# Kernel optimization log

Hardware: AMD Instinct MI355X
Metric: run time of the kernel (lower is better)

The kernel has to match this reference:

```python
import jax, jax.numpy as jnp
import numpy as np

N = 100_000      # nodes
E = 3_200_000    # directed edges (avg degree 32)
F_IN = 503
C = 32           # GATConv out_channels, heads=1
NEG_SLOPE = 0.2  # PyG GATConv default


def setup_inputs() -> dict:
    key = jax.random.key(0)
    ks = jax.random.split(key, 14)
    x = jax.random.normal(ks[0], (N, F_IN), jnp.float32)
    edge_index = jax.random.randint(ks[1], (2, E), 0, N)
    edge_weight = jax.random.uniform(ks[2], (E, 1), jnp.float32)
    input_mask = jnp.ones((N, 1), jnp.float32)
    # GATConv params (heads=1)
    W_src = jax.random.normal(ks[3], (C, F_IN), jnp.float32) * 0.02
    att_src = jax.random.normal(ks[4], (C,), jnp.float32) * 0.1
    att_dst = jax.random.normal(ks[5], (C,), jnp.float32) * 0.1
    att_edge = jax.random.normal(ks[6], (C,), jnp.float32) * 0.1
    W_edge = jax.random.normal(ks[7], (C, 1), jnp.float32) * 0.1
    bias_conv = jnp.zeros((C,), jnp.float32)
    # dense heads
    Wb = jax.random.normal(ks[8], (1, C), jnp.float32) * 0.1
    bb = jnp.zeros((1,), jnp.float32)
    Ww = jax.random.normal(ks[9], (1, C), jnp.float32) * 0.1
    bw = jnp.zeros((1,), jnp.float32)
    return {"x": x, "edge_index": edge_index, "edge_weight": edge_weight,
            "input_mask": input_mask, "W_src": W_src, "att_src": att_src,
            "att_dst": att_dst, "att_edge": att_edge, "W_edge": W_edge,
            "bias_conv": bias_conv, "Wb": Wb, "bb": bb, "Ww": Ww, "bw": bw}


def reference(x, edge_index, edge_weight, input_mask, W_src, att_src, att_dst,
              att_edge, W_edge, bias_conv, Wb, bb, Ww, bw):
    n = x.shape[0]
    xl = x @ W_src.T                       # [N, C] transformed node features
    a_src = xl @ att_src                   # [N] per-node source attention logit
    a_dst = xl @ att_dst                   # [N]
    src, dst = edge_index[0], edge_index[1]
    # add_self_loops=True with fill_value='mean' for edge_attr (PyG default)
    loop = jnp.arange(n)
    mean_attr = jnp.mean(edge_weight, axis=0, keepdims=True)      # [1,1]
    ea = jnp.concatenate([edge_weight, jnp.broadcast_to(mean_attr, (n, 1))], 0)
    s = jnp.concatenate([src, loop])       # [E+N]
    d = jnp.concatenate([dst, loop])
    a_edge = (ea @ W_edge.T) @ att_edge    # [E+N]
    alpha = jax.nn.leaky_relu(a_src[s] + a_dst[d] + a_edge, NEG_SLOPE)
    # softmax over incoming edges of each destination node
    amax = jax.ops.segment_max(alpha, d, num_segments=n)
    ex = jnp.exp(alpha - amax[d])
    denom = jax.ops.segment_sum(ex, d, num_segments=n)
    w = ex / denom[d]                      # [E+N] attention coeffs
    msg = xl[s] * w[:, None]               # [E+N, C]
    out = jax.ops.segment_sum(msg, d, num_segments=n) + bias_conv  # [N, C]
    h = jax.nn.relu(out)
    biases = (h @ Wb.T + bb) * input_mask  # [N, 1]
    weights = ((h[src] + h[dst]) * 0.5) @ Ww.T + bw  # [E, 1]
    return weights, biases
```

## Files before the change

### kernel.cpp

```cpp
#include <hip/hip_runtime.h>
#include <stdint.h>

#define NN 100000
#define NE 3200000
#define FIN 503
#define COUT 32
#define NSLOPE 0.2f

#define BSH 6
#define NB 1563
#define HB 256
#define EPB (NE / HB)
#define MAXBE 2560

typedef __bf16 bf16x8 __attribute__((ext_vector_type(8)));
typedef float  f32x4  __attribute__((ext_vector_type(4)));

__device__ __forceinline__ unsigned short bf1(float f) {
    unsigned u = __float_as_uint(f);
    u = (u + 0x7FFFu + ((u >> 16) & 1u)) >> 16;
    return (unsigned short)u;
}
__device__ __forceinline__ unsigned bf2(float a, float b) {
    return (unsigned)bf1(a) | ((unsigned)bf1(b) << 16);
}
__device__ __forceinline__ float unbf(unsigned short h) {
    return __uint_as_float(((unsigned)h) << 16);
}

__global__ void k_wprep(const float* __restrict__ W, uint4* __restrict__ wfrag)
{
    int entry = blockIdx.x * 256 + threadIdx.x;
    if (entry >= 2048) return;
    int c = entry & 31;
    int quad = (entry >> 5) & 3;
    int chunk = entry >> 7;
    int kb = chunk * 32 + quad * 8;
    float v[8];
    #pragma unroll
    for (int j = 0; j < 8; ++j) {
        int k = kb + j;
        v[j] = (k < FIN) ? W[c * FIN + k] : 0.f;
    }
    uint4 o;
    o.x = bf2(v[0], v[1]); o.y = bf2(v[2], v[3]);
    o.z = bf2(v[4], v[5]); o.w = bf2(v[6], v[7]);
    wfrag[entry] = o;
}

#define GR 64

__global__ __launch_bounds__(256)
void k_gemm(const float* __restrict__ x, const uint4* __restrict__ wfrag,
            unsigned short* __restrict__ xlb)
{
    __shared__ __align__(16) unsigned short os[GR * 40];
    const int t = threadIdx.x;
    const int wv = t >> 6, lane = t & 63;
    const int m16 = lane & 15, quad = lane >> 4;
    const int row0 = blockIdx.x * GR;
    const int row = row0 + wv * 16 + m16;
    const int rowc = (row < NN) ? row : (NN - 1);
    const float* xr = x + (size_t)rowc * FIN;

    f32x4 acc0 = {0.f, 0.f, 0.f, 0.f};
    f32x4 acc1 = {0.f, 0.f, 0.f, 0.f};

    #pragma unroll 5
    for (int ch = 0; ch < 15; ++ch) {
        const int kb = ch * 32 + quad * 8;
        float av[8];
        #pragma unroll
        for (int j = 0; j < 8; ++j) av[j] = xr[kb + j];
        bf16x8 af;
        #pragma unroll
        for (int j = 0; j < 8; ++j) af[j] = (__bf16)av[j];
        uint4 b0 = wfrag[ch * 128 + quad * 32 + m16];
        uint4 b1 = wfrag[ch * 128 + quad * 32 + 16 + m16];
        acc0 = __builtin_amdgcn_mfma_f32_16x16x32_bf16(af, *(bf16x8*)&b0, acc0, 0, 0, 0);
        acc1 = __builtin_amdgcn_mfma_f32_16x16x32_bf16(af, *(bf16x8*)&b1, acc1, 0, 0, 0);
    }
    {
        const int kb = 480 + quad * 8;
        float av[8];
        #pragma unroll
        for (int j = 0; j < 8; ++j) av[j] = (kb + j < FIN) ? xr[kb + j] : 0.f;
        bf16x8 af;
        #pragma unroll
        for (int j = 0; j < 8; ++j) af[j] = (__bf16)av[j];
        uint4 b0 = wfrag[15 * 128 + quad * 32 + m16];
        uint4 b1 = wfrag[15 * 128 + quad * 32 + 16 + m16];
        acc0 = __builtin_amdgcn_mfma_f32_16x16x32_bf16(af, *(bf16x8*)&b0, acc0, 0, 0, 0);
        acc1 = __builtin_amdgcn_mfma_f32_16x16x32_bf16(af, *(bf16x8*)&b1, acc1, 0, 0, 0);
    }

    #pragma unroll
    for (int r = 0; r < 4; ++r) {
        int rr = wv * 16 + quad * 4 + r;
        os[rr * 40 + m16]      = bf1(acc0[r]);
        os[rr * 40 + 16 + m16] = bf1(acc1[r]);
    }
    __syncthreads();
    {
        int r = t >> 2, c0 = (t & 3) * 8;
        int grow = row0 + r;
        if (grow < NN) {
            uint4 o = *(const uint4*)&os[r * 40 + c0];
            *(uint4*)&xlb[(size_t)grow * COUT + c0] = o;
        }
    }
}

__global__ void k_attn(const unsigned short* __restrict__ xlb,
                       const float* __restrict__ att_s, const float* __restrict__ att_d,
                       float* __restrict__ a_src, float* __restrict__ a_dst)
{
    int n = blockIdx.x * 256 + threadIdx.x;
    if (n >= NN) return;
    const unsigned short* r = xlb + (size_t)n * COUT;
    float s = 0.f, d = 0.f;
    #pragma unroll
    for (int c = 0; c < COUT; c += 2) {
        unsigned u = *(const unsigned*)&r[c];
        float v0 = __uint_as_float(u << 16);
        float v1 = __uint_as_float(u & 0xFFFF0000u);
        s += v0 * att_s[c] + v1 * att_s[c + 1];
        d += v0 * att_d[c] + v1 * att_d[c + 1];
    }
    a_src[n] = s; a_dst[n] = d;
}

__global__ void k_stats(const float* __restrict__ ew, const float* __restrict__ W_edge,
                        const float* __restrict__ att_e, float* __restrict__ stats)
{
    float s = 0.f;
    for (int i = blockIdx.x * blockDim.x + threadIdx.x; i < NE; i += gridDim.x * blockDim.x)
        s += ew[i];
    #pragma unroll
    for (int off = 32; off > 0; off >>= 1) s += __shfl_xor(s, off);
    if ((threadIdx.x & 63) == 0) atomicAdd(&stats[0], s);
    if (blockIdx.x == 0 && threadIdx.x == 0) {
        float k = 0.f;
        for (int c = 0; c < COUT; ++c) k += W_edge[c] * att_e[c];
        stats[1] = k;
    }
}

__global__ __launch_bounds__(512)
void k_hist(const int* __restrict__ ei_dst, unsigned* __restrict__ part)
{
    __shared__ unsigned h[NB];
    for (int i = threadIdx.x; i < NB; i += 512) h[i] = 0u;
    __syncthreads();
    const int base = blockIdx.x * EPB;
    for (int i = threadIdx.x; i < EPB; i += 512)
        atomicAdd(&h[ei_dst[base + i] >> BSH], 1u);
    __syncthreads();
    for (int i = threadIdx.x; i < NB; i += 512)
        part[(size_t)blockIdx.x * NB + i] = h[i];
}

__global__ void k_colscan(unsigned* __restrict__ part, unsigned* __restrict__ colsum)
{
    __shared__ unsigned sm[HB];
    const int t = threadIdx.x;
    const int bkt = blockIdx.x;
    unsigned v = part[(size_t)t * NB + bkt];
    sm[t] = v;
    for (int off = 1; off < HB; off <<= 1) {
        __syncthreads();
        unsigned tv = (t >= off) ? sm[t - off] : 0u;
        __syncthreads();
        sm[t] += tv;
    }
    __syncthreads();
    part[(size_t)t * NB + bkt] = sm[t] - v;
    if (t == HB - 1) colsum[bkt] = sm[t];
}

__global__ void k_bscan(const unsigned* __restrict__ colsum, unsigned* __restrict__ bbase)
{
    __shared__ unsigned sm[256];
    __shared__ unsigned carry;
    const int t = threadIdx.x;
    if (t == 0) carry = 0u;
    __syncthreads();
    for (int c0 = 0; c0 < NB; c0 += 256) {
        int i = c0 + t;
        unsigned v = (i < NB) ? colsum[i] : 0u;
        sm[t] = v;
        for (int off = 1; off < 256; off <<= 1) {
            __syncthreads();
            unsigned tv = (t >= off) ? sm[t - off] : 0u;
            __syncthreads();
            sm[t] += tv;
        }
        __syncthreads();
        if (i < NB) bbase[i] = carry + sm[t] - v;
        __syncthreads();
        if (t == 0) carry += sm[255];
        __syncthreads();
    }
    if (t == 0) bbase[NB] = carry;
}

__global__ __launch_bounds__(512)
void k_scatter(const int* __restrict__ ei, const float* __restrict__ ew,
               const float* __restrict__ a_src, const float* __restrict__ stats,
               const unsigned* __restrict__ part, const unsigned* __restrict__ bbase,
               uint2* __restrict__ csr)
{
    __shared__ unsigned cur[NB];
    const int b = blockIdx.x;
    for (int i = threadIdx.x; i < NB; i += 512)
        cur[i] = bbase[i] + part[(size_t)b * NB + i];
    __syncthreads();
    const float kc = stats[1];
    const int base = b * EPB;
    for (int i = threadIdx.x; i < EPB; i += 512) {
        int e = base + i;
        int s = ei[e];
        int d = ei[NE + e];
        float pre = a_src[s] + kc * ew[e];
        unsigned pos = atomicAdd(&cur[d >> BSH], 1u);
        csr[pos] = make_uint2((unsigned)s | ((unsigned)(d & 63) << 20),
                              __float_as_uint(pre));
    }
}

__global__ __launch_bounds__(256)
void k_aggr(const uint2* __restrict__ csr, const unsigned* __restrict__ bbase,
            const float* __restrict__ a_src, const float* __restrict__ a_dst,
            const unsigned short* __restrict__ xlb, const float* __restrict__ stats,
            const float* __restrict__ bias_conv, const float* __restrict__ Wb,
            const float* __restrict__ bb, const float* __restrict__ Ww,
            const float* __restrict__ mask, float* __restrict__ out_b,
            float* __restrict__ hw)
{
    __shared__ uint2 rec[MAXBE];
    __shared__ unsigned seg[65], cur[64];
    const int t = threadIdx.x;
    const int b = blockIdx.x;
    const int jb = (int)bbase[b];
    int ne = (int)bbase[b + 1] - jb;
    if (ne > MAXBE) ne = MAXBE;

    if (t < 64) cur[t] = 0u;
    __syncthreads();
    for (int i = t; i < ne; i += 256)
        atomicAdd(&cur[csr[jb + i].x >> 20], 1u);
    __syncthreads();
    if (t < 64) {
        unsigned v = cur[t];
        unsigned s = v;
        #pragma unroll
        for (int off = 1; off < 64; off <<= 1) {
            unsigned u = __shfl_up(s, off, 64);
            if (t >= off) s += u;
        }
        seg[t + 1] = s;
        cur[t] = s - v;
        if (t == 0) seg[0] = 0u;
    }
    __syncthreads();
    for (int i = t; i < ne; i += 256) {
        uint2 r = csr[jb + i];
        unsigned pos = atomicAdd(&cur[r.x >> 20], 1u);
        rec[pos] = r;
    }
    __syncthreads();

    const float kmean = stats[1] * (stats[0] * (1.f / NE));
    const int lane = t & 31;
    for (int dl = t >> 5; dl < 64; dl += 8) {
        int d = (b << BSH) + dl;
        if (d >= NN) continue;
        const float adv = a_dst[d];
        float a0 = a_src[d] + adv + kmean;
        a0 = (a0 > 0.f) ? a0 : NSLOPE * a0;
        const float ps = __expf(a0);
        float l = 0.f;
        float acc = ps * unbf(xlb[(size_t)d * COUT + lane]);
        const int j0 = (int)seg[dl], j1 = (int)seg[dl + 1];
        for (int tb = j0; tb < j1; tb += 32) {
            int j = tb + lane;
            float p = 0.f;
            if (j < j1) {
                uint2 en = rec[j];
                float a = __uint_as_float(en.y) + adv;
                a = (a > 0.f) ? a : NSLOPE * a;
                p = __expf(a);
                rec[j].y = __float_as_uint(p);
            }
            l += p;
            int cnte = min(32, j1 - tb);
            #pragma unroll 4
            for (int k = 0; k < cnte; ++k) {
                uint2 en = rec[tb + k];
                acc += __uint_as_float(en.y) *
                       unbf(xlb[(size_t)(en.x & 0xFFFFFu) * COUT + lane]);
            }
        }
        #pragma unroll
        for (int off = 16; off > 0; off >>= 1) l += __shfl_xor(l, off, 32);
        l += ps;
        float h = fmaxf(acc / l + bias_conv[lane], 0.f);
        float pb = h * Wb[lane];
        float pw = h * Ww[lane];
        #pragma unroll
        for (int off = 16; off > 0; off >>= 1) {
            pb += __shfl_xor(pb, off, 32);
            pw += __shfl_xor(pw, off, 32);
        }
        if (lane == 0) {
            out_b[d] = (pb + bb[0]) * mask[d];
            hw[d] = pw;
        }
    }
}

__global__ void k_weights(const int* __restrict__ ei, const float* __restrict__ hw,
                          const float* __restrict__ bw, float* __restrict__ out_w)
{
    int e = blockIdx.x * 256 + threadIdx.x;
    if (e < NE) {
        int s = ei[e], d = ei[NE + e];
        out_w[e] = 0.5f * (hw[s] + hw[d]) + bw[0];
    }
}

extern "C" void kernel_launch(void* const* d_in, const int* in_sizes, int n_in,
                              void* d_out, int out_size, void* d_ws, size_t ws_size,
                              hipStream_t stream)
{
    const float* x        = (const float*)d_in[0];
    const int*   ei       = (const int*)d_in[1];
    const float* ew       = (const float*)d_in[2];
    const float* mask     = (const float*)d_in[3];
    const float* W_src    = (const float*)d_in[4];
    const float* att_src  = (const float*)d_in[5];
    const float* att_dst  = (const float*)d_in[6];
    const float* att_edge = (const float*)d_in[7];
    const float* W_edge   = (const float*)d_in[8];
    const float* bias_c   = (const float*)d_in[9];
    const float* Wb       = (const float*)d_in[10];
    const float* bb       = (const float*)d_in[11];
    const float* Ww       = (const float*)d_in[12];
    const float* bw       = (const float*)d_in[13];
    (void)in_sizes; (void)n_in; (void)out_size; (void)ws_size;

    char* wsp = (char*)d_ws;
    size_t off = 0;
    auto alloc = [&](size_t bytes) -> void* {
        void* p = wsp + off;
        off = (off + bytes + 255) & ~(size_t)255;
        return p;
    };
    unsigned short* xlb    = (unsigned short*)alloc((size_t)NN * COUT * 2);
    uint4*    wfrag  = (uint4*)alloc(2048 * 16);
    float*    a_src  = (float*)alloc((size_t)NN * 4);
    float*    a_dst  = (float*)alloc((size_t)NN * 4);
    float*    stats  = (float*)alloc(256);
    unsigned* part   = (unsigned*)alloc((size_t)HB * NB * 4);
    unsigned* colsum = (unsigned*)alloc((size_t)NB * 4);
    unsigned* bbase  = (unsigned*)alloc((size_t)(NB + 1) * 4);
    uint2*    csr    = (uint2*)alloc((size_t)NE * 8);
    float*    hw     = (float*)alloc((size_t)NN * 4);

    float* out_w = (float*)d_out;
    float* out_b = out_w + NE;

    hipMemsetAsync(stats, 0, 8, stream);

    k_wprep   <<<8, 256, 0, stream>>>(W_src, wfrag);
    k_gemm    <<<(NN + GR - 1) / GR, 256, 0, stream>>>(x, wfrag, xlb);
    k_attn    <<<(NN + 255) / 256, 256, 0, stream>>>(xlb, att_src, att_dst, a_src, a_dst);
    k_stats   <<<1024, 256, 0, stream>>>(ew, W_edge, att_edge, stats);
    k_hist    <<<HB, 512, 0, stream>>>(ei + NE, part);
    k_colscan <<<NB, HB, 0, stream>>>(part, colsum);
    k_bscan   <<<1, 256, 0, stream>>>(colsum, bbase);
    k_scatter <<<HB, 512, 0, stream>>>(ei, ew, a_src, stats, part, bbase, csr);
    k_aggr    <<<NB, 256, 0, stream>>>(csr, bbase, a_src, a_dst, xlb, stats,
                                       bias_c, Wb, bb, Ww, mask, out_b, hw);
    k_weights <<<NE / 256, 256, 0, stream>>>(ei, hw, bw, out_w);
}
```

Before: 583.8 us.

## Fuse prep kernels, stage GEMM input through LDS, register-cache CSR records

Merges weight-fragment prep into the edge-weight reduction kernel, which now writes per-block partial sums instead of using atomics and a memset. The final reduction and the attention constant move into the single-block bucket scan. The node-attention dot products are folded into the GEMM epilogue, and GEMM input rows are staged through shared memory with coalesced loads. The aggregation kernel keeps its CSR records in registers instead of reading them twice. The goal is fewer launches and less redundant global traffic, at the cost of extra barriers in the GEMM loop and more register pressure in the aggregation kernel.

Measured after the change: 530.9 us. 1.1x faster.

```diff
diff --git a/kernel.cpp b/kernel.cpp
--- a/kernel.cpp
+++ b/kernel.cpp
@@ -12,6 +12,7 @@
 #define HB 256
 #define EPB (NE / HB)
 #define MAXBE 2560
+#define NREG (MAXBE / 256)
 
 typedef __bf16 bf16x8 __attribute__((ext_vector_type(8)));
 typedef float  f32x4  __attribute__((ext_vector_type(4)));
@@ -28,50 +29,78 @@
     return __uint_as_float(((unsigned)h) << 16);
 }
 
-__global__ void k_wprep(const float* __restrict__ W, uint4* __restrict__ wfrag)
-{
-    int entry = blockIdx.x * 256 + threadIdx.x;
-    if (entry >= 2048) return;
-    int c = entry & 31;
-    int quad = (entry >> 5) & 3;
-    int chunk = entry >> 7;
-    int kb = chunk * 32 + quad * 8;
-    float v[8];
+__global__ __launch_bounds__(256)
+void k_stats(const float* __restrict__ ew, float* __restrict__ partial,
+             const float* __restrict__ W, uint4* __restrict__ wfrag)
+{
+    const int t = threadIdx.x;
+    const int gid = blockIdx.x * 256 + t;
+
+    if (gid < 2048) {
+        int c = gid & 31;
+        int quad = (gid >> 5) & 3;
+        int chunk = gid >> 7;
+        int kb = chunk * 32 + quad * 8;
+        float v[8];
+        #pragma unroll
+        for (int j = 0; j < 8; ++j) {
+            int k = kb + j;
+            v[j] = (k < FIN) ? W[c * FIN + k] : 0.f;
+        }
+        uint4 o;
+        o.x = bf2(v[0], v[1]); o.y = bf2(v[2], v[3]);
+        o.z = bf2(v[4], v[5]); o.w = bf2(v[6], v[7]);
+        wfrag[gid] = o;
+    }
+
+    const float4* ew4 = (const float4*)ew;
+    float s = 0.f;
+    for (int i = gid; i < NE / 4; i += gridDim.x * 256) {
+        float4 v = ew4[i];
+        s += v.x + v.y + v.z + v.w;
+    }
     #pragma unroll
-    for (int j = 0; j < 8; ++j) {
-        int k = kb + j;
-        v[j] = (k < FIN) ? W[c * FIN + k] : 0.f;
-    }
-    uint4 o;
-    o.x = bf2(v[0], v[1]); o.y = bf2(v[2], v[3]);
-    o.z = bf2(v[4], v[5]); o.w = bf2(v[6], v[7]);
-    wfrag[entry] = o;
+    for (int off = 32; off > 0; off >>= 1) s += __shfl_xor(s, off);
+    __shared__ float wsum[4];
+    if ((t & 63) == 0) wsum[t >> 6] = s;
+    __syncthreads();
+    if (t == 0) partial[blockIdx.x] = wsum[0] + wsum[1] + wsum[2] + wsum[3];
 }
 
 #define GR 64
 
 __global__ __launch_bounds__(256)
 void k_gemm(const float* __restrict__ x, const uint4* __restrict__ wfrag,
-            unsigned short* __restrict__ xlb)
-{
+            const float* __restrict__ att_s, const float* __restrict__ att_d,
+            unsigned short* __restrict__ xlb,
+            float* __restrict__ a_src, float* __restrict__ a_dst)
+{
+    __shared__ __align__(16) float xs[GR][36];
     __shared__ __align__(16) unsigned short os[GR * 40];
     const int t = threadIdx.x;
     const int wv = t >> 6, lane = t & 63;
     const int m16 = lane & 15, quad = lane >> 4;
     const int row0 = blockIdx.x * GR;
-    const int row = row0 + wv * 16 + m16;
-    const int rowc = (row < NN) ? row : (NN - 1);
-    const float* xr = x + (size_t)rowc * FIN;
+    const int srow = t >> 5;
+    const int scol = t & 31;
 
     f32x4 acc0 = {0.f, 0.f, 0.f, 0.f};
     f32x4 acc1 = {0.f, 0.f, 0.f, 0.f};
-
-    #pragma unroll 5
-    for (int ch = 0; ch < 15; ++ch) {
-        const int kb = ch * 32 + quad * 8;
+    const int rowf = wv * 16 + m16;
+
+    for (int ch = 0; ch < 16; ++ch) {
+        const int k = ch * 32 + scol;
+        #pragma unroll
+        for (int p = 0; p < 8; ++p) {
+            int r = p * 8 + srow;
+            int rg = row0 + r;
+            rg = (rg < NN) ? rg : (NN - 1);
+            xs[r][scol] = (k < FIN) ? x[(size_t)rg * FIN + k] : 0.f;
+        }
+        __syncthreads();
         float av[8];
-        #pragma unroll
-        for (int j = 0; j < 8; ++j) av[j] = xr[kb + j];
+        *(f32x4*)&av[0] = *(const f32x4*)&xs[rowf][quad * 8];
+        *(f32x4*)&av[4] = *(const f32x4*)&xs[rowf][quad * 8 + 4];
         bf16x8 af;
         #pragma unroll
         for (int j = 0; j < 8; ++j) af[j] = (__bf16)av[j];
@@ -79,19 +108,7 @@
         uint4 b1 = wfrag[ch * 128 + quad * 32 + 16 + m16];
         acc0 = __builtin_amdgcn_mfma_f32_16x16x32_bf16(af, *(bf16x8*)&b0, acc0, 0, 0, 0);
         acc1 = __builtin_amdgcn_mfma_f32_16x16x32_bf16(af, *(bf16x8*)&b1, acc1, 0, 0, 0);
-    }
-    {
-        const int kb = 480 + quad * 8;
-        float av[8];
-        #pragma unroll
-        for (int j = 0; j < 8; ++j) av[j] = (kb + j < FIN) ? xr[kb + j] : 0.f;
-        bf16x8 af;
-        #pragma unroll
-        for (int j = 0; j < 8; ++j) af[j] = (__bf16)av[j];
-        uint4 b0 = wfrag[15 * 128 + quad * 32 + m16];
-        uint4 b1 = wfrag[15 * 128 + quad * 32 + 16 + m16];
-        acc0 = __builtin_amdgcn_mfma_f32_16x16x32_bf16(af, *(bf16x8*)&b0, acc0, 0, 0, 0);
-        acc1 = __builtin_amdgcn_mfma_f32_16x16x32_bf16(af, *(bf16x8*)&b1, acc1, 0, 0, 0);
+        __syncthreads();
     }
 
     #pragma unroll
@@ -104,45 +121,21 @@
     {
         int r = t >> 2, c0 = (t & 3) * 8;
         int grow = row0 + r;
+        uint4 o = *(const uint4*)&os[r * 40 + c0];
+        float s = 0.f, dd = 0.f;
+        const unsigned short* oh = (const unsigned short*)&o;
+        #pragma unroll
+        for (int j = 0; j < 8; ++j) {
+            float v = unbf(oh[j]);
+            s  += v * att_s[c0 + j];
+            dd += v * att_d[c0 + j];
+        }
+        s  += __shfl_xor(s, 1, 4);  s  += __shfl_xor(s, 2, 4);
+        dd += __shfl_xor(dd, 1, 4); dd += __shfl_xor(dd, 2, 4);
         if (grow < NN) {
-            uint4 o = *(const uint4*)&os[r * 40 + c0];
             *(uint4*)&xlb[(size_t)grow * COUT + c0] = o;
-        }
-    }
-}
-
-__global__ void k_attn(const unsigned short* __restrict__ xlb,
-                       const float* __restrict__ att_s, const float* __restrict__ att_d,
-                       float* __restrict__ a_src, float* __restrict__ a_dst)
-{
-    int n = blockIdx.x * 256 + threadIdx.x;
-    if (n >= NN) return;
-    const unsigned short* r = xlb + (size_t)n * COUT;
-    float s = 0.f, d = 0.f;
-    #pragma unroll
-    for (int c = 0; c < COUT; c += 2) {
-        unsigned u = *(const unsigned*)&r[c];
-        float v0 = __uint_as_float(u << 16);
-        float v1 = __uint_as_float(u & 0xFFFF0000u);
-        s += v0 * att_s[c] + v1 * att_s[c + 1];
-        d += v0 * att_d[c] + v1 * att_d[c + 1];
-    }
-    a_src[n] = s; a_dst[n] = d;
-}
-
-__global__ void k_stats(const float* __restrict__ ew, const float* __restrict__ W_edge,
-                        const float* __restrict__ att_e, float* __restrict__ stats)
-{
-    float s = 0.f;
-    for (int i = blockIdx.x * blockDim.x + threadIdx.x; i < NE; i += gridDim.x * blockDim.x)
-        s += ew[i];
-    #pragma unroll
-    for (int off = 32; off > 0; off >>= 1) s += __shfl_xor(s, off);
-    if ((threadIdx.x & 63) == 0) atomicAdd(&stats[0], s);
-    if (blockIdx.x == 0 && threadIdx.x == 0) {
-        float k = 0.f;
-        for (int c = 0; c < COUT; ++c) k += W_edge[c] * att_e[c];
-        stats[1] = k;
+            if ((t & 3) == 0) { a_src[grow] = s; a_dst[grow] = dd; }
+        }
     }
 }
 
@@ -178,11 +171,31 @@
     if (t == HB - 1) colsum[bkt] = sm[t];
 }
 
-__global__ void k_bscan(const unsigned* __restrict__ colsum, unsigned* __restrict__ bbase)
-{
+__global__ void k_bscan(const unsigned* __restrict__ colsum, unsigned* __restrict__ bbase,
+                        const float* __restrict__ partial, const float* __restrict__ W_edge,
+                        const float* __restrict__ att_e, float* __restrict__ stats)
+{
+    const int t = threadIdx.x;
+    {
+        __shared__ float fs[256];
+        float ps = partial[t] + partial[t + 256] + partial[t + 512] + partial[t + 768];
+        fs[t] = ps;
+        __syncthreads();
+        for (int off = 128; off > 0; off >>= 1) {
+            if (t < off) fs[t] += fs[t + off];
+            __syncthreads();
+        }
+        if (t == 0) {
+            stats[0] = fs[0];
+            float k = 0.f;
+            for (int c = 0; c < COUT; ++c) k += W_edge[c] * att_e[c];
+            stats[1] = k;
+        }
+    }
+    __syncthreads();
+
     __shared__ unsigned sm[256];
     __shared__ unsigned carry;
-    const int t = threadIdx.x;
     if (t == 0) carry = 0u;
     __syncthreads();
     for (int c0 = 0; c0 < NB; c0 += 256) {
@@ -245,10 +258,17 @@
     int ne = (int)bbase[b + 1] - jb;
     if (ne > MAXBE) ne = MAXBE;
 
+    uint2 rg[NREG];
+    #pragma unroll
+    for (int j = 0; j < NREG; ++j) {
+        int i = t + j * 256;
+        rg[j] = (i < ne) ? csr[jb + i] : make_uint2(0u, 0u);
+    }
     if (t < 64) cur[t] = 0u;
     __syncthreads();
-    for (int i = t; i < ne; i += 256)
-        atomicAdd(&cur[csr[jb + i].x >> 20], 1u);
+    #pragma unroll
+    for (int j = 0; j < NREG; ++j)
+        if (t + j * 256 < ne) atomicAdd(&cur[rg[j].x >> 20], 1u);
     __syncthreads();
     if (t < 64) {
         unsigned v = cur[t];
@@ -263,11 +283,12 @@
         if (t == 0) seg[0] = 0u;
     }
     __syncthreads();
-    for (int i = t; i < ne; i += 256) {
-        uint2 r = csr[jb + i];
-        unsigned pos = atomicAdd(&cur[r.x >> 20], 1u);
-        rec[pos] = r;
-    }
+    #pragma unroll
+    for (int j = 0; j < NREG; ++j)
+        if (t + j * 256 < ne) {
+            unsigned pos = atomicAdd(&cur[rg[j].x >> 20], 1u);
+            rec[pos] = rg[j];
+        }
     __syncthreads();
 
     const float kmean = stats[1] * (stats[0] * (1.f / NE));
@@ -361,6 +382,7 @@
     float*    a_src  = (float*)alloc((size_t)NN * 4);
     float*    a_dst  = (float*)alloc((size_t)NN * 4);
     float*    stats  = (float*)alloc(256);
+    float*    partial= (float*)alloc(1024 * 4);
     unsigned* part   = (unsigned*)alloc((size_t)HB * NB * 4);
     unsigned* colsum = (unsigned*)alloc((size_t)NB * 4);
     unsigned* bbase  = (unsigned*)alloc((size_t)(NB + 1) * 4);
@@ -370,15 +392,12 @@
     float* out_w = (float*)d_out;
     float* out_b = out_w + NE;
 
-    hipMemsetAsync(stats, 0, 8, stream);
-
-    k_wprep   <<<8, 256, 0, stream>>>(W_src, wfrag);
-    k_gemm    <<<(NN + GR - 1) / GR, 256, 0, stream>>>(x, wfrag, xlb);
-    k_attn    <<<(NN + 255) / 256, 256, 0, stream>>>(xlb, att_src, att_dst, a_src, a_dst);
-    k_stats   <<<1024, 256, 0, stream>>>(ew, W_edge, att_edge, stats);
+    k_stats   <<<1024, 256, 0, stream>>>(ew, partial, W_src, wfrag);
+    k_gemm    <<<(NN + GR - 1) / GR, 256, 0, stream>>>(x, wfrag, att_src, att_dst,
+                                                       xlb, a_src, a_dst);
     k_hist    <<<HB, 512, 0, stream>>>(ei + NE, part);
     k_colscan <<<NB, HB, 0, stream>>>(part, colsum);
-    k_bscan   <<<1, 256, 0, stream>>>(colsum, bbase);
+    k_bscan   <<<1, 256, 0, stream>>>(colsum, bbase, partial, W_edge, att_edge, stats);
     k_scatter <<<HB, 512, 0, stream>>>(ei, ew, a_src, stats, part, bbase, csr);
     k_aggr    <<<NB, 256, 0, stream>>>(csr, bbase, a_src, a_dst, xlb, stats,
                                        bias_c, Wb, bb, Ww, mask, out_b, hw);
```
